# Kernel optimization log

Hardware: AMD Instinct MI355X
Metric: run time of the kernel (lower is better)

The kernel has to match this reference:

```python
import jax, jax.numpy as jnp
import numpy as np

# Closed-over physics constants (forward_model scalar args)
L = 1.0
SIGMA = 0.14
R_FILM0 = 50.0
VR = 1.0
DT = 0.1
NT = 2000
SCALE = 1e9  # sigmoid sharpness used by limit/tradeoff
B = 4096
NODES = 64


def setup_inputs() -> dict:
    key = jax.random.key(0)
    ks = jax.random.split(key, 9)
    Cv = jax.random.uniform(ks[0], (B,), jnp.float32) * 0.5 + 0.1
    K = jax.random.uniform(ks[1], (B,), jnp.float32) * 1.0 + 0.5
    jmin = jax.random.uniform(ks[2], (B,), jnp.float32) * 0.01
    W1 = jax.random.normal(ks[3], (1, NODES), jnp.float32) * 0.3
    b1 = jax.random.normal(ks[4], (NODES,), jnp.float32) * 0.1
    W2 = jax.random.normal(ks[5], (NODES, NODES), jnp.float32) * 0.1
    b2 = jax.random.normal(ks[6], (NODES,), jnp.float32) * 0.1
    W3 = jax.random.normal(ks[7], (NODES, 1), jnp.float32) * 0.1
    b3 = jax.random.normal(ks[8], (1,), jnp.float32) * 0.1
    return {"Cv": Cv, "K": K, "jmin": jmin, "W1": W1, "b1": b1,
            "W2": W2, "b2": b2, "W3": W3, "b3": b3}


def _limit(val, lim, scale):
    # (val-lim)/(1+exp(-scale*(val-lim))) + lim
    d = val - lim
    return d * jax.nn.sigmoid(scale * d) + lim


def _tradeoff(val1, val2, coord, lim, scale):
    return (val1 - val2) * jax.nn.sigmoid(scale * (coord - lim)) + val2


def reference(Cv, K, jmin, W1, b1, W2, b2, W3, b3):
    b = Cv.shape[0]
    beta = SIGMA * VR / (SIGMA * R_FILM0 + L)
    Qmin = (81.0 / (128.0 * beta)) ** (1.0 / 3.0) * K ** (4.0 / 3.0)  # (b,)

    def rho_mlp(j):  # j: (b,) -> (b,)
        h = jax.nn.relu(j[:, None] @ W1 + b1)
        h = jax.nn.relu(h @ W2 + b2)
        return (h @ W3 + b3)[:, 0]

    def step(carry, i):
        res, thk, Q = carry  # each (b,)
        BC = VR * DT * (i + 1).astype(jnp.float32)
        jcur = SIGMA * BC / (SIGMA * res + L)
        Qn = Q + jcur * DT
        rho = rho_mlp(jcur)
        thk_n = _tradeoff(_limit(thk + Cv * (jcur - jmin) * DT, 0.0, SCALE),
                          thk, Qn, Qmin, SCALE)
        res_n = _tradeoff(_limit(res + rho * (jcur - jmin) * DT * Cv, R_FILM0, SCALE),
                          res, Qn, Qmin, SCALE)
        return (res_n, thk_n, Qn), (res_n, thk_n, jcur)

    res0 = jnp.full((b,), R_FILM0, jnp.float32)
    thk0 = jnp.zeros((b,), jnp.float32)
    Q0 = jnp.zeros((b,), jnp.float32)
    _, (res_seq, thk_seq, j_seq) = jax.lax.scan(
        step, (res0, thk0, Q0), jnp.arange(NT - 1))
    # seqs: (nt-1, b) -> full (b, nt)
    resistance = jnp.concatenate([res0[None, :], res_seq], 0).T
    thickness = jnp.concatenate([thk0[None, :], thk_seq], 0).T
    current = jnp.concatenate([jnp.full((1, b), 1e-3, jnp.float32), j_seq], 0).T
    time = jnp.broadcast_to(DT * jnp.arange(NT, dtype=jnp.float32), (b, NT))
    return (thickness[..., None], resistance[..., None], current[..., None], time)
```

## Files before the change

### kernel.cpp

```cpp
#include <hip/hip_runtime.h>

#define NT      2000
#define BATCH   4096
#define NODES   64
#define TBL_N   8192
#define JMAX    3.6f
#define ENTB    (TBL_N / 4)
#define NCB     (BATCH / 256)
#define FILLB   (BATCH * NT / 4 / 256)
#define MAXIT   24
#define CHUNKS  ((NT + 255) / 256)

template<int CTRL, int RMASK>
__device__ __forceinline__ float updpp(float oldv, float x) {
    return __int_as_float(__builtin_amdgcn_update_dpp(
        __float_as_int(oldv), __float_as_int(x), CTRL, RMASK, 0xF, false));
}
__device__ __forceinline__ float rdl63(float v) {
    return __int_as_float(__builtin_amdgcn_readlane(__float_as_int(v), 63));
}
__device__ __forceinline__ float rdl(float v, int k) {
    return __int_as_float(__builtin_amdgcn_readlane(__float_as_int(v), k));
}

__device__ __forceinline__ void scan_sc(float& S, float& C) {
    const float NI = -3.0e38f;
    float Su, Cu;
    Su = updpp<0x111, 0xF>(0.0f, S); Cu = updpp<0x111, 0xF>(NI, C);
    C = fmaxf(Cu + S, C); S = Su + S;
    Su = updpp<0x112, 0xF>(0.0f, S); Cu = updpp<0x112, 0xF>(NI, C);
    C = fmaxf(Cu + S, C); S = Su + S;
    Su = updpp<0x114, 0xF>(0.0f, S); Cu = updpp<0x114, 0xF>(NI, C);
    C = fmaxf(Cu + S, C); S = Su + S;
    Su = updpp<0x118, 0xF>(0.0f, S); Cu = updpp<0x118, 0xF>(NI, C);
    C = fmaxf(Cu + S, C); S = Su + S;
    Su = updpp<0x142, 0xA>(0.0f, S); Cu = updpp<0x142, 0xA>(NI, C);
    C = fmaxf(Cu + S, C); S = Su + S;
    Su = updpp<0x143, 0xC>(0.0f, S); Cu = updpp<0x143, 0xC>(NI, C);
    C = fmaxf(Cu + S, C); S = Su + S;
}

__device__ __forceinline__ float scan_add(float S) {
    float Su;
    Su = updpp<0x111, 0xF>(0.0f, S); S += Su;
    Su = updpp<0x112, 0xF>(0.0f, S); S += Su;
    Su = updpp<0x114, 0xF>(0.0f, S); S += Su;
    Su = updpp<0x118, 0xF>(0.0f, S); S += Su;
    Su = updpp<0x142, 0xA>(0.0f, S); S += Su;
    Su = updpp<0x143, 0xC>(0.0f, S); S += Su;
    return S;
}

__global__ __launch_bounds__(256) void prep(
    const float* __restrict__ W1, const float* __restrict__ b1,
    const float* __restrict__ W2, const float* __restrict__ b2,
    const float* __restrict__ W3, const float* __restrict__ b3,
    const float* __restrict__ K,
    float* __restrict__ tbl, int* __restrict__ ncArr,
    float* __restrict__ out) {
    if (blockIdx.x < ENTB) {
        const int lane = threadIdx.x & 63;
        const int idx = blockIdx.x * 4 + (threadIdx.x >> 6);
        const float h = JMAX / (float)TBL_N;
        const float j = h * (float)idx;

        float h1 = fmaxf(fmaf(j, W1[lane], b1[lane]), 0.0f);

        float acc = b2[lane];
#pragma unroll
        for (int k = 0; k < NODES; ++k) {
            float h1k = rdl(h1, k);
            acc = fmaf(h1k, W2[k * NODES + lane], acc);
        }
        float p = fmaxf(acc, 0.0f) * W3[lane];

        float rho = rdl63(scan_add(p)) + b3[0];
        if (lane == 0) tbl[idx] = rho;
    } else if (blockIdx.x < ENTB + NCB) {
        int b = (blockIdx.x - ENTB) * 256 + threadIdx.x;
        float Qmin = 3.3068376f * powf(K[b], 1.3333334f);
        int nc = 1 << 20;
        float Q = 0.0f;
        for (int o = 1; o <= 360; ++o) {
            float BC = 0.1f * (float)o;
            float jc = (0.14f * BC) * 0.125f;
            Q = fmaf(jc, 0.1f, Q);
            if (Q > Qmin) { nc = o; break; }
        }
        ncArr[b] = min(nc, NT - 1);
    } else {
        int e = (blockIdx.x - ENTB - NCB) * 256 + threadIdx.x;
        int t0 = (e * 4) % NT;
        float4 v = make_float4(0.1f * (float)t0, 0.1f * (float)(t0 + 1),
                               0.1f * (float)(t0 + 2), 0.1f * (float)(t0 + 3));
        reinterpret_cast<float4*>(out + 3 * (size_t)BATCH * NT)[e] = v;
    }
}

__global__ __launch_bounds__(64, 4) void fused(
    const float* __restrict__ Cv, const float* __restrict__ jmin,
    const int* __restrict__ ncArr, const float* __restrict__ tbl,
    float* __restrict__ out) {
    const float NI = -3.0e38f;
    const int lane = threadIdx.x;
    const int b = blockIdx.x;
    const float cv = Cv[b];
    const float jm = jmin[b];
    const int   nc = ncArr[b];
    const float k1    = cv * 0.1f;
    const float nk1jm = -k1 * jm;
    const float invh  = (float)TBL_N / JMAX;

    float* __restrict__ oT  = out + (size_t)b * NT;
    float* __restrict__ oR  = out + (size_t)BATCH * NT + (size_t)b * NT;
    float* __restrict__ oC  = out + 2 * (size_t)BATCH * NT + (size_t)b * NT;

    float carry = 50.0f, slope = 0.0f, curv = 0.0f;
    float y = 0.0f;

    for (int c = 0; c < CHUNKS; ++c) {
        const int ob = c << 8;
        const int o0 = ob + 4 * lane, o1 = o0 + 1, o2 = o0 + 2, o3 = o0 + 3;
        const int q = (ob >> 2) + lane;

        if (ob + 255 < nc) {
            float j0 = (o0 == 0) ? 1e-3f : 0.00175f * (float)o0;
            reinterpret_cast<float4*>(oT)[q] = make_float4(0.f, 0.f, 0.f, 0.f);
            reinterpret_cast<float4*>(oR)[q] = make_float4(50.f, 50.f, 50.f, 50.f);
            reinterpret_cast<float4*>(oC)[q] = make_float4(
                j0, 0.00175f * (float)o1, 0.00175f * (float)o2,
                0.00175f * (float)o3);
            continue;
        }

        const float tm0 = 0.1f * (float)o0, tm1 = 0.1f * (float)o1;
        const float tm2 = 0.1f * (float)o2, tm3 = 0.1f * (float)o3;
        const float co0 = 0.14f * tm0, co1 = 0.14f * tm1;
        const float co2 = 0.14f * tm2, co3 = 0.14f * tm3;
        const bool a0 = (o0 >= nc) && (o0 < NT);
        const bool a1 = (o1 >= nc) && (o1 < NT);
        const bool a2 = (o2 >= nc) && (o2 < NT);
        const bool a3 = (o3 >= nc) && (o3 < NT);

        const float s0 = (float)(4 * lane + 1);
        float g0 = fmaf(fmaf(curv, s0, slope), s0, carry);
        const float s1 = s0 + 1.0f;
        float g1 = fmaf(fmaf(curv, s1, slope), s1, carry);
        const float s2 = s0 + 2.0f;
        float g2 = fmaf(fmaf(curv, s2, slope), s2, carry);
        const float s3 = s0 + 3.0f;
        float g3 = fmaf(fmaf(curv, s3, slope), s3, carry);

        float j0, j1, j2, j3, n0, n1, n2, n3;
        for (int it = 0; it < MAXIT; ++it) {
            float rp0 = updpp<0x138, 0xF>(carry, g3);
            float rp1 = g0, rp2 = g1, rp3 = g2;
            j0 = co0 * __builtin_amdgcn_rcpf(fmaf(0.14f, rp0, 1.0f));
            j1 = co1 * __builtin_amdgcn_rcpf(fmaf(0.14f, rp1, 1.0f));
            j2 = co2 * __builtin_amdgcn_rcpf(fmaf(0.14f, rp2, 1.0f));
            j3 = co3 * __builtin_amdgcn_rcpf(fmaf(0.14f, rp3, 1.0f));

            float x0 = fminf(fmaxf(j0 * invh, 0.0f), (float)(TBL_N - 2));
            float x1 = fminf(fmaxf(j1 * invh, 0.0f), (float)(TBL_N - 2));
            float x2 = fminf(fmaxf(j2 * invh, 0.0f), (float)(TBL_N - 2));
            float x3 = fminf(fmaxf(j3 * invh, 0.0f), (float)(TBL_N - 2));
            int ip0 = (int)x0, ip1 = (int)x1, ip2 = (int)x2, ip3 = (int)x3;
            float fr0 = x0 - (float)ip0, fr1 = x1 - (float)ip1;
            float fr2 = x2 - (float)ip2, fr3 = x3 - (float)ip3;
            float ta0 = tbl[ip0], tb0 = tbl[ip0 + 1];
            float ta1 = tbl[ip1], tb1 = tbl[ip1 + 1];
            float ta2 = tbl[ip2], tb2 = tbl[ip2 + 1];
            float ta3 = tbl[ip3], tb3 = tbl[ip3 + 1];
            float rho0 = fmaf(fr0, tb0 - ta0, ta0);
            float rho1 = fmaf(fr1, tb1 - ta1, ta1);
            float rho2 = fmaf(fr2, tb2 - ta2, ta2);
            float rho3 = fmaf(fr3, tb3 - ta3, ta3);

            n0 = fmaf(k1, j0, nk1jm); n1 = fmaf(k1, j1, nk1jm);
            n2 = fmaf(k1, j2, nk1jm); n3 = fmaf(k1, j3, nk1jm);
            float i0 = a0 ? rho0 * n0 : 0.0f;
            float i1 = a1 ? rho1 * n1 : 0.0f;
            float i2 = a2 ? rho2 * n2 : 0.0f;
            float i3 = a3 ? rho3 * n3 : 0.0f;
            float c0 = a0 ? 50.0f : NI, c1 = a1 ? 50.0f : NI;
            float c2 = a2 ? 50.0f : NI, c3 = a3 ? 50.0f : NI;

            float LS0 = i0,        LC0 = c0;
            float LS1 = LS0 + i1,  LC1 = fmaxf(LC0 + i1, c1);
            float LS2 = LS1 + i2,  LC2 = fmaxf(LC1 + i2, c2);
            float LS3 = LS2 + i3,  LC3 = fmaxf(LC2 + i3, c3);

            float Sw = LS3, Cw = LC3;
            scan_sc(Sw, Cw);
            float Se = updpp<0x138, 0xF>(0.0f, Sw);
            float Ce = updpp<0x138, 0xF>(NI, Cw);

            float r0 = fmaxf(carry + (Se + LS0), fmaxf(Ce + LS0, LC0));
            float r1 = fmaxf(carry + (Se + LS1), fmaxf(Ce + LS1, LC1));
            float r2 = fmaxf(carry + (Se + LS2), fmaxf(Ce + LS2, LC2));
            float r3 = fmaxf(carry + (Se + LS3), fmaxf(Ce + LS3, LC3));

            float d = fmaxf(fmaxf(fabsf(r0 - g0), fabsf(r1 - g1)),
                            fmaxf(fabsf(r2 - g2), fabsf(r3 - g3)));
            g0 = r0; g1 = r1; g2 = r2; g3 = r3;
            if (__all(d <= 1.0e-3f)) break;
        }

        {
            float i0 = a0 ? n0 : 0.0f, i1 = a1 ? n1 : 0.0f;
            float i2 = a2 ? n2 : 0.0f, i3 = a3 ? n3 : 0.0f;
            float c0 = a0 ? 0.0f : NI, c1 = a1 ? 0.0f : NI;
            float c2 = a2 ? 0.0f : NI, c3 = a3 ? 0.0f : NI;
            float LS0 = i0,        LC0 = c0;
            float LS1 = LS0 + i1,  LC1 = fmaxf(LC0 + i1, c1);
            float LS2 = LS1 + i2,  LC2 = fmaxf(LC1 + i2, c2);
            float LS3 = LS2 + i3,  LC3 = fmaxf(LC2 + i3, c3);
            float Sw = LS3, Cw = LC3;
            scan_sc(Sw, Cw);
            float Se = updpp<0x138, 0xF>(0.0f, Sw);
            float Ce = updpp<0x138, 0xF>(NI, Cw);
            float t0 = fmaxf(y + (Se + LS0), fmaxf(Ce + LS0, LC0));
            float t1 = fmaxf(y + (Se + LS1), fmaxf(Ce + LS1, LC1));
            float t2 = fmaxf(y + (Se + LS2), fmaxf(Ce + LS2, LC2));
            float t3 = fmaxf(y + (Se + LS3), fmaxf(Ce + LS3, LC3));

            if (o0 == 0) j0 = 1e-3f;

            if (o3 < NT) {
                reinterpret_cast<float4*>(oT)[q] = make_float4(t0, t1, t2, t3);
                reinterpret_cast<float4*>(oR)[q] = make_float4(g0, g1, g2, g3);
                reinterpret_cast<float4*>(oC)[q] = make_float4(j0, j1, j2, j3);
            }
            y = rdl63(t3);
        }

        float lastR = rdl63(g3);
        float ns = (lastR - carry) * 0.00390625f;
        curv = (ns - slope) * 0.001953125f;
        slope = ns;
        carry = lastR;
    }
}

extern "C" void kernel_launch(void* const* d_in, const int* in_sizes, int n_in,
                              void* d_out, int out_size, void* d_ws, size_t ws_size,
                              hipStream_t stream) {
    const float* Cv   = (const float*)d_in[0];
    const float* K    = (const float*)d_in[1];
    const float* jmin = (const float*)d_in[2];
    const float* W1   = (const float*)d_in[3];
    const float* b1   = (const float*)d_in[4];
    const float* W2   = (const float*)d_in[5];
    const float* b2   = (const float*)d_in[6];
    const float* W3   = (const float*)d_in[7];
    const float* b3   = (const float*)d_in[8];
    float* out = (float*)d_out;
    float* tbl = (float*)d_ws;
    int*   ncA = (int*)((char*)d_ws + TBL_N * sizeof(float));

    prep<<<ENTB + NCB + FILLB, 256, 0, stream>>>(
        W1, b1, W2, b2, W3, b3, K, tbl, ncA, out);
    fused<<<BATCH, 64, 0, stream>>>(Cv, jmin, ncA, tbl, out);
}
```

Before: 44.05 us.

## Store value-delta table pairs, fast-path plain scan, move time fill into fused kernel

```diff
diff --git a/kernel.cpp b/kernel.cpp
--- a/kernel.cpp
+++ b/kernel.cpp
@@ -7,7 +7,6 @@
 #define JMAX    3.6f
 #define ENTB    (TBL_N / 4)
 #define NCB     (BATCH / 256)
-#define FILLB   (BATCH * NT / 4 / 256)
 #define MAXIT   24
 #define CHUNKS  ((NT + 255) / 256)
 
@@ -56,27 +55,32 @@
     const float* __restrict__ W2, const float* __restrict__ b2,
     const float* __restrict__ W3, const float* __restrict__ b3,
     const float* __restrict__ K,
-    float* __restrict__ tbl, int* __restrict__ ncArr,
-    float* __restrict__ out) {
+    float2* __restrict__ tbl, int* __restrict__ ncArr) {
     if (blockIdx.x < ENTB) {
         const int lane = threadIdx.x & 63;
         const int idx = blockIdx.x * 4 + (threadIdx.x >> 6);
         const float h = JMAX / (float)TBL_N;
-        const float j = h * (float)idx;
-
-        float h1 = fmaxf(fmaf(j, W1[lane], b1[lane]), 0.0f);
-
-        float acc = b2[lane];
+        const float ja = h * (float)idx;
+        const float jb = ja + h;
+
+        float w1 = W1[lane], bb1 = b1[lane];
+        float h1a = fmaxf(fmaf(ja, w1, bb1), 0.0f);
+        float h1b = fmaxf(fmaf(jb, w1, bb1), 0.0f);
+
+        float acca = b2[lane], accb = acca;
 #pragma unroll
         for (int k = 0; k < NODES; ++k) {
-            float h1k = rdl(h1, k);
-            acc = fmaf(h1k, W2[k * NODES + lane], acc);
-        }
-        float p = fmaxf(acc, 0.0f) * W3[lane];
-
-        float rho = rdl63(scan_add(p)) + b3[0];
-        if (lane == 0) tbl[idx] = rho;
-    } else if (blockIdx.x < ENTB + NCB) {
+            float w2 = W2[k * NODES + lane];
+            acca = fmaf(rdl(h1a, k), w2, acca);
+            accb = fmaf(rdl(h1b, k), w2, accb);
+        }
+        float w3 = W3[lane];
+        float pa = fmaxf(acca, 0.0f) * w3;
+        float pb = fmaxf(accb, 0.0f) * w3;
+        float rhoa = rdl63(scan_add(pa)) + b3[0];
+        float rhob = rdl63(scan_add(pb)) + b3[0];
+        if (lane == 0) tbl[idx] = make_float2(rhoa, rhob - rhoa);
+    } else {
         int b = (blockIdx.x - ENTB) * 256 + threadIdx.x;
         float Qmin = 3.3068376f * powf(K[b], 1.3333334f);
         int nc = 1 << 20;
@@ -88,18 +92,12 @@
             if (Q > Qmin) { nc = o; break; }
         }
         ncArr[b] = min(nc, NT - 1);
-    } else {
-        int e = (blockIdx.x - ENTB - NCB) * 256 + threadIdx.x;
-        int t0 = (e * 4) % NT;
-        float4 v = make_float4(0.1f * (float)t0, 0.1f * (float)(t0 + 1),
-                               0.1f * (float)(t0 + 2), 0.1f * (float)(t0 + 3));
-        reinterpret_cast<float4*>(out + 3 * (size_t)BATCH * NT)[e] = v;
     }
 }
 
 __global__ __launch_bounds__(64, 4) void fused(
     const float* __restrict__ Cv, const float* __restrict__ jmin,
-    const int* __restrict__ ncArr, const float* __restrict__ tbl,
+    const int* __restrict__ ncArr, const float2* __restrict__ tbl,
     float* __restrict__ out) {
     const float NI = -3.0e38f;
     const int lane = threadIdx.x;
@@ -114,6 +112,7 @@
     float* __restrict__ oT  = out + (size_t)b * NT;
     float* __restrict__ oR  = out + (size_t)BATCH * NT + (size_t)b * NT;
     float* __restrict__ oC  = out + 2 * (size_t)BATCH * NT + (size_t)b * NT;
+    float* __restrict__ oTm = out + 3 * (size_t)BATCH * NT + (size_t)b * NT;
 
     float carry = 50.0f, slope = 0.0f, curv = 0.0f;
     float y = 0.0f;
@@ -122,16 +121,6 @@
         const int ob = c << 8;
         const int o0 = ob + 4 * lane, o1 = o0 + 1, o2 = o0 + 2, o3 = o0 + 3;
         const int q = (ob >> 2) + lane;
-
-        if (ob + 255 < nc) {
-            float j0 = (o0 == 0) ? 1e-3f : 0.00175f * (float)o0;
-            reinterpret_cast<float4*>(oT)[q] = make_float4(0.f, 0.f, 0.f, 0.f);
-            reinterpret_cast<float4*>(oR)[q] = make_float4(50.f, 50.f, 50.f, 50.f);
-            reinterpret_cast<float4*>(oC)[q] = make_float4(
-                j0, 0.00175f * (float)o1, 0.00175f * (float)o2,
-                0.00175f * (float)o3);
-            continue;
-        }
 
         const float tm0 = 0.1f * (float)o0, tm1 = 0.1f * (float)o1;
         const float tm2 = 0.1f * (float)o2, tm3 = 0.1f * (float)o3;
@@ -154,27 +143,21 @@
         float j0, j1, j2, j3, n0, n1, n2, n3;
         for (int it = 0; it < MAXIT; ++it) {
             float rp0 = updpp<0x138, 0xF>(carry, g3);
-            float rp1 = g0, rp2 = g1, rp3 = g2;
             j0 = co0 * __builtin_amdgcn_rcpf(fmaf(0.14f, rp0, 1.0f));
-            j1 = co1 * __builtin_amdgcn_rcpf(fmaf(0.14f, rp1, 1.0f));
-            j2 = co2 * __builtin_amdgcn_rcpf(fmaf(0.14f, rp2, 1.0f));
-            j3 = co3 * __builtin_amdgcn_rcpf(fmaf(0.14f, rp3, 1.0f));
+            j1 = co1 * __builtin_amdgcn_rcpf(fmaf(0.14f, g0, 1.0f));
+            j2 = co2 * __builtin_amdgcn_rcpf(fmaf(0.14f, g1, 1.0f));
+            j3 = co3 * __builtin_amdgcn_rcpf(fmaf(0.14f, g2, 1.0f));
 
             float x0 = fminf(fmaxf(j0 * invh, 0.0f), (float)(TBL_N - 2));
             float x1 = fminf(fmaxf(j1 * invh, 0.0f), (float)(TBL_N - 2));
             float x2 = fminf(fmaxf(j2 * invh, 0.0f), (float)(TBL_N - 2));
             float x3 = fminf(fmaxf(j3 * invh, 0.0f), (float)(TBL_N - 2));
             int ip0 = (int)x0, ip1 = (int)x1, ip2 = (int)x2, ip3 = (int)x3;
-            float fr0 = x0 - (float)ip0, fr1 = x1 - (float)ip1;
-            float fr2 = x2 - (float)ip2, fr3 = x3 - (float)ip3;
-            float ta0 = tbl[ip0], tb0 = tbl[ip0 + 1];
-            float ta1 = tbl[ip1], tb1 = tbl[ip1 + 1];
-            float ta2 = tbl[ip2], tb2 = tbl[ip2 + 1];
-            float ta3 = tbl[ip3], tb3 = tbl[ip3 + 1];
-            float rho0 = fmaf(fr0, tb0 - ta0, ta0);
-            float rho1 = fmaf(fr1, tb1 - ta1, ta1);
-            float rho2 = fmaf(fr2, tb2 - ta2, ta2);
-            float rho3 = fmaf(fr3, tb3 - ta3, ta3);
+            float2 vd0 = tbl[ip0], vd1 = tbl[ip1], vd2 = tbl[ip2], vd3 = tbl[ip3];
+            float rho0 = fmaf(x0 - (float)ip0, vd0.y, vd0.x);
+            float rho1 = fmaf(x1 - (float)ip1, vd1.y, vd1.x);
+            float rho2 = fmaf(x2 - (float)ip2, vd2.y, vd2.x);
+            float rho3 = fmaf(x3 - (float)ip3, vd3.y, vd3.x);
 
             n0 = fmaf(k1, j0, nk1jm); n1 = fmaf(k1, j1, nk1jm);
             n2 = fmaf(k1, j2, nk1jm); n3 = fmaf(k1, j3, nk1jm);
@@ -182,23 +165,32 @@
             float i1 = a1 ? rho1 * n1 : 0.0f;
             float i2 = a2 ? rho2 * n2 : 0.0f;
             float i3 = a3 ? rho3 * n3 : 0.0f;
-            float c0 = a0 ? 50.0f : NI, c1 = a1 ? 50.0f : NI;
-            float c2 = a2 ? 50.0f : NI, c3 = a3 ? 50.0f : NI;
-
-            float LS0 = i0,        LC0 = c0;
-            float LS1 = LS0 + i1,  LC1 = fmaxf(LC0 + i1, c1);
-            float LS2 = LS1 + i2,  LC2 = fmaxf(LC1 + i2, c2);
-            float LS3 = LS2 + i3,  LC3 = fmaxf(LC2 + i3, c3);
-
-            float Sw = LS3, Cw = LC3;
-            scan_sc(Sw, Cw);
-            float Se = updpp<0x138, 0xF>(0.0f, Sw);
-            float Ce = updpp<0x138, 0xF>(NI, Cw);
-
-            float r0 = fmaxf(carry + (Se + LS0), fmaxf(Ce + LS0, LC0));
-            float r1 = fmaxf(carry + (Se + LS1), fmaxf(Ce + LS1, LC1));
-            float r2 = fmaxf(carry + (Se + LS2), fmaxf(Ce + LS2, LC2));
-            float r3 = fmaxf(carry + (Se + LS3), fmaxf(Ce + LS3, LC3));
+
+            float LS0 = i0, LS1 = LS0 + i1, LS2 = LS1 + i2, LS3 = LS2 + i3;
+
+            float Sp = scan_add(LS3);
+            float Se = updpp<0x138, 0xF>(0.0f, Sp);
+            float r0 = carry + (Se + LS0);
+            float r1 = carry + (Se + LS1);
+            float r2 = carry + (Se + LS2);
+            float r3 = carry + (Se + LS3);
+            float mn = fminf(fminf(r0, r1), fminf(r2, r3));
+            if (!__all(mn >= 50.0f)) {
+                float c0 = a0 ? 50.0f : NI, c1 = a1 ? 50.0f : NI;
+                float c2 = a2 ? 50.0f : NI, c3 = a3 ? 50.0f : NI;
+                float LC0 = c0;
+                float LC1 = fmaxf(LC0 + i1, c1);
+                float LC2 = fmaxf(LC1 + i2, c2);
+                float LC3 = fmaxf(LC2 + i3, c3);
+                float Sw = LS3, Cw = LC3;
+                scan_sc(Sw, Cw);
+                float Sx = updpp<0x138, 0xF>(0.0f, Sw);
+                float Cx = updpp<0x138, 0xF>(NI, Cw);
+                r0 = fmaxf(carry + (Sx + LS0), fmaxf(Cx + LS0, LC0));
+                r1 = fmaxf(carry + (Sx + LS1), fmaxf(Cx + LS1, LC1));
+                r2 = fmaxf(carry + (Sx + LS2), fmaxf(Cx + LS2, LC2));
+                r3 = fmaxf(carry + (Sx + LS3), fmaxf(Cx + LS3, LC3));
+            }
 
             float d = fmaxf(fmaxf(fabsf(r0 - g0), fabsf(r1 - g1)),
                             fmaxf(fabsf(r2 - g2), fabsf(r3 - g3)));
@@ -209,27 +201,21 @@
         {
             float i0 = a0 ? n0 : 0.0f, i1 = a1 ? n1 : 0.0f;
             float i2 = a2 ? n2 : 0.0f, i3 = a3 ? n3 : 0.0f;
-            float c0 = a0 ? 0.0f : NI, c1 = a1 ? 0.0f : NI;
-            float c2 = a2 ? 0.0f : NI, c3 = a3 ? 0.0f : NI;
-            float LS0 = i0,        LC0 = c0;
-            float LS1 = LS0 + i1,  LC1 = fmaxf(LC0 + i1, c1);
-            float LS2 = LS1 + i2,  LC2 = fmaxf(LC1 + i2, c2);
-            float LS3 = LS2 + i3,  LC3 = fmaxf(LC2 + i3, c3);
-            float Sw = LS3, Cw = LC3;
-            scan_sc(Sw, Cw);
-            float Se = updpp<0x138, 0xF>(0.0f, Sw);
-            float Ce = updpp<0x138, 0xF>(NI, Cw);
-            float t0 = fmaxf(y + (Se + LS0), fmaxf(Ce + LS0, LC0));
-            float t1 = fmaxf(y + (Se + LS1), fmaxf(Ce + LS1, LC1));
-            float t2 = fmaxf(y + (Se + LS2), fmaxf(Ce + LS2, LC2));
-            float t3 = fmaxf(y + (Se + LS3), fmaxf(Ce + LS3, LC3));
+            float LS0 = i0, LS1 = LS0 + i1, LS2 = LS1 + i2, LS3 = LS2 + i3;
+            float Sp = scan_add(LS3);
+            float Se = updpp<0x138, 0xF>(0.0f, Sp);
+            float t0 = y + (Se + LS0);
+            float t1 = y + (Se + LS1);
+            float t2 = y + (Se + LS2);
+            float t3 = y + (Se + LS3);
 
             if (o0 == 0) j0 = 1e-3f;
 
             if (o3 < NT) {
-                reinterpret_cast<float4*>(oT)[q] = make_float4(t0, t1, t2, t3);
-                reinterpret_cast<float4*>(oR)[q] = make_float4(g0, g1, g2, g3);
-                reinterpret_cast<float4*>(oC)[q] = make_float4(j0, j1, j2, j3);
+                reinterpret_cast<float4*>(oT)[q]  = make_float4(t0, t1, t2, t3);
+                reinterpret_cast<float4*>(oR)[q]  = make_float4(g0, g1, g2, g3);
+                reinterpret_cast<float4*>(oC)[q]  = make_float4(j0, j1, j2, j3);
+                reinterpret_cast<float4*>(oTm)[q] = make_float4(tm0, tm1, tm2, tm3);
             }
             y = rdl63(t3);
         }
@@ -255,10 +241,9 @@
     const float* W3   = (const float*)d_in[7];
     const float* b3   = (const float*)d_in[8];
     float* out = (float*)d_out;
-    float* tbl = (float*)d_ws;
-    int*   ncA = (int*)((char*)d_ws + TBL_N * sizeof(float));
-
-    prep<<<ENTB + NCB + FILLB, 256, 0, stream>>>(
-        W1, b1, W2, b2, W3, b3, K, tbl, ncA, out);
+    float2* tbl = (float2*)d_ws;
+    int*    ncA = (int*)((char*)d_ws + TBL_N * sizeof(float2));
+
+    prep<<<ENTB + NCB, 256, 0, stream>>>(W1, b1, W2, b2, W3, b3, K, tbl, ncA);
     fused<<<BATCH, 64, 0, stream>>>(Cv, jmin, ncA, tbl, out);
 }
```

Result: slower. 45.88 us (+4.2%).
